# Performance work log

Hardware: AMD Instinct MI355X
Metric: run time of the kernel (lower is better)

Reference implementation:

```python
import jax, jax.numpy as jnp
import numpy as np


def setup_inputs() -> dict:
    key = jax.random.key(0)
    ks = jax.random.split(key, 6)
    L, B, S, D = 2, 32, 2048, 1024
    dec_hidden = jax.random.normal(ks[0], (L, B, D), dtype=jnp.float32)
    enc_out = jax.random.normal(ks[1], (B, S, D), dtype=jnp.float32)
    mask = jax.random.randint(ks[2], (B, S), 0, 2, dtype=jnp.int32)
    sc = 1.0 / np.sqrt(D)
    W_dec = jax.random.normal(ks[3], (D, D), dtype=jnp.float32) * sc
    W_enc = jax.random.normal(ks[4], (D, D), dtype=jnp.float32) * sc
    w_att = jax.random.normal(ks[5], (D, 1), dtype=jnp.float32) * sc
    return {
        "decoder_hidden": dec_hidden,
        "encoder_outputs": enc_out,
        "mask": mask,
        "W_dec": W_dec,
        "b_dec": jnp.zeros((D,), jnp.float32),
        "W_enc": W_enc,
        "b_enc": jnp.zeros((D,), jnp.float32),
        "w_att": w_att,
        "b_att": jnp.zeros((1,), jnp.float32),
    }


def reference(decoder_hidden, encoder_outputs, mask, W_dec, b_dec, W_enc, b_enc, w_att, b_att):
    # decoder_hidden: [L, B, Dd] -> take last layer, project to enc dim: [B, 1, De]
    dec_proj = decoder_hidden[-1] @ W_dec + b_dec            # [B, De]
    enc_proj = jnp.einsum("bse,ef->bsf", encoder_outputs, W_enc) + b_enc  # [B, S, De]
    energy = jnp.tanh(dec_proj[:, None, :] + enc_proj)        # [B, S, De]
    scores = jnp.einsum("bse,eo->bso", energy, w_att)[..., 0] + b_att[0]  # [B, S]
    scores = jnp.where(mask == 0, jnp.float32(-1e10), scores)
    attn = jax.nn.softmax(scores, axis=1)                     # [B, S]
    context = jnp.einsum("bs,bse->be", attn, encoder_outputs)[:, None, :]  # [B, 1, De]
    return context, attn
```

## Files before the change

### kernel.cpp

```cpp
#include <hip/hip_runtime.h>
#include <hip/hip_bf16.h>

constexpr int LAY = 2;
constexpr int BB  = 32;
constexpr int SS  = 2048;
constexpr int DD  = 1024;

typedef unsigned short u16;
typedef short  short8  __attribute__((ext_vector_type(8)));
typedef u16    u16x8   __attribute__((ext_vector_type(8)));
typedef float  floatx4 __attribute__((ext_vector_type(4)));

__device__ inline u16 f2bf_rn(float f) {
    union { float f; unsigned int i; } v; v.f = f;
    unsigned int x = v.i;
    return (u16)((x + 0x7FFFu + ((x >> 16) & 1u)) >> 16);
}

__global__ void transpose_wenc(const float* __restrict__ W, u16* __restrict__ wT) {
    int idx = blockIdx.x * 256 + threadIdx.x;
    int k = idx >> 10, n = idx & 1023;
    wT[n * DD + k] = f2bf_rn(W[idx]);
}

__global__ __launch_bounds__(256) void dec_proj_kernel(
    const float* __restrict__ dec_hidden, const float* __restrict__ W_dec,
    const float* __restrict__ b_dec, float* __restrict__ dec_proj) {
    int b = blockIdx.x, t = threadIdx.x;
    const float* h = dec_hidden + (LAY - 1) * BB * DD + b * DD;
    float acc0 = 0.f, acc1 = 0.f, acc2 = 0.f, acc3 = 0.f;
    for (int e = 0; e < DD; ++e) {
        float hv = h[e];
        const float* wr = W_dec + e * DD;
        acc0 += hv * wr[t];
        acc1 += hv * wr[t + 256];
        acc2 += hv * wr[t + 512];
        acc3 += hv * wr[t + 768];
    }
    float* dp = dec_proj + b * DD;
    dp[t]       = acc0 + b_dec[t];
    dp[t + 256] = acc1 + b_dec[t + 256];
    dp[t + 512] = acc2 + b_dec[t + 512];
    dp[t + 768] = acc3 + b_dec[t + 768];
}

constexpr int LDK = 72;

__global__ __launch_bounds__(256) void score_gemm(
    const float* __restrict__ enc,
    const u16*   __restrict__ wT,
    const float* __restrict__ dec_proj,
    const float* __restrict__ b_enc, const float* __restrict__ w_att,
    float* __restrict__ scores) {
    __shared__ u16 As[128 * LDK];
    __shared__ u16 Bs[128 * LDK];

    const int tid  = threadIdx.x;
    const int bn   = blockIdx.x;
    const int bm   = blockIdx.y;
    const int row0 = bm * 128, col0 = bn * 128;
    const int lane = tid & 63, w = tid >> 6;
    const int wm   = w >> 1,  wn = w & 1;
    const int quad = lane >> 4, l16 = lane & 15;

    const int pr = tid >> 3;
    const int pc = (tid & 7) * 8;

    floatx4 acc[4][4];
    #pragma unroll
    for (int i = 0; i < 4; ++i)
        #pragma unroll
        for (int j = 0; j < 4; ++j)
            acc[i][j] = (floatx4){0.f, 0.f, 0.f, 0.f};

    for (int kt = 0; kt < DD / 64; ++kt) {
        const int k0 = kt * 64;
        floatx4 af0[4], af1[4];
        u16x8 bv[4];
        #pragma unroll
        for (int i = 0; i < 4; ++i) {
            int r = pr + i * 32;
            const float* src = enc + (size_t)(row0 + r) * DD + k0 + pc;
            af0[i] = *reinterpret_cast<const floatx4*>(src);
            af1[i] = *reinterpret_cast<const floatx4*>(src + 4);
            bv[i]  = *reinterpret_cast<const u16x8*>(&wT[(size_t)(col0 + r) * DD + k0 + pc]);
        }
        __syncthreads();
        #pragma unroll
        for (int i = 0; i < 4; ++i) {
            int r = pr + i * 32;
            u16x8 a8;
            #pragma unroll
            for (int j = 0; j < 4; ++j) {
                a8[j]     = f2bf_rn(af0[i][j]);
                a8[4 + j] = f2bf_rn(af1[i][j]);
            }
            *reinterpret_cast<u16x8*>(&As[r * LDK + pc]) = a8;
            *reinterpret_cast<u16x8*>(&Bs[r * LDK + pc]) = bv[i];
        }
        __syncthreads();
        #pragma unroll
        for (int ks = 0; ks < 2; ++ks) {
            short8 a[4], b[4];
            #pragma unroll
            for (int tm = 0; tm < 4; ++tm)
                a[tm] = *reinterpret_cast<const short8*>(
                    &As[(wm * 64 + tm * 16 + l16) * LDK + ks * 32 + quad * 8]);
            #pragma unroll
            for (int tn = 0; tn < 4; ++tn)
                b[tn] = *reinterpret_cast<const short8*>(
                    &Bs[(wn * 64 + tn * 16 + l16) * LDK + ks * 32 + quad * 8]);
            #pragma unroll
            for (int tm = 0; tm < 4; ++tm)
                #pragma unroll
                for (int tn = 0; tn < 4; ++tn)
                    acc[tm][tn] = __builtin_amdgcn_mfma_f32_16x16x32_bf16(
                        a[tm], b[tn], acc[tm][tn], 0, 0, 0);
        }
        __syncthreads();
    }

    const int bIdx = row0 / SS;
    const float* dp = dec_proj + bIdx * DD;
    float cvec[4], wvv[4];
    #pragma unroll
    for (int tn = 0; tn < 4; ++tn) {
        int n = col0 + wn * 64 + tn * 16 + l16;
        cvec[tn] = dp[n] + b_enc[n];
        wvv[tn]  = w_att[n];
    }
    #pragma unroll
    for (int tm = 0; tm < 4; ++tm) {
        float rs0 = 0.f, rs1 = 0.f, rs2 = 0.f, rs3 = 0.f;
        #pragma unroll
        for (int tn = 0; tn < 4; ++tn) {
            rs0 += tanhf(acc[tm][tn][0] + cvec[tn]) * wvv[tn];
            rs1 += tanhf(acc[tm][tn][1] + cvec[tn]) * wvv[tn];
            rs2 += tanhf(acc[tm][tn][2] + cvec[tn]) * wvv[tn];
            rs3 += tanhf(acc[tm][tn][3] + cvec[tn]) * wvv[tn];
        }
        #pragma unroll
        for (int off = 1; off < 16; off <<= 1) {
            rs0 += __shfl_xor(rs0, off, 64);
            rs1 += __shfl_xor(rs1, off, 64);
            rs2 += __shfl_xor(rs2, off, 64);
            rs3 += __shfl_xor(rs3, off, 64);
        }
        if (l16 == 0) {
            int rbase = row0 + wm * 64 + tm * 16 + quad * 4;
            atomicAdd(&scores[rbase + 0], rs0);
            atomicAdd(&scores[rbase + 1], rs1);
            atomicAdd(&scores[rbase + 2], rs2);
            atomicAdd(&scores[rbase + 3], rs3);
        }
    }
}

__global__ __launch_bounds__(256) void softmax_kernel(
    const float* __restrict__ scores, const int* __restrict__ mask,
    float* __restrict__ attn_out) {
    int b = blockIdx.x, t = threadIdx.x;
    const float* srow = scores + b * SS;
    const int*   mrow = mask + b * SS;
    float vals[8];
    float vmax = -1e30f;
    #pragma unroll
    for (int i = 0; i < 8; ++i) {
        int s = i * 256 + t;
        float v = (mrow[s] == 0) ? -1e10f : srow[s];
        vals[i] = v;
        vmax = fmaxf(vmax, v);
    }
    #pragma unroll
    for (int off = 32; off >= 1; off >>= 1) vmax = fmaxf(vmax, __shfl_xor(vmax, off, 64));
    __shared__ float sm[4];
    if ((t & 63) == 0) sm[t >> 6] = vmax;
    __syncthreads();
    vmax = fmaxf(fmaxf(sm[0], sm[1]), fmaxf(sm[2], sm[3]));
    float sum = 0.f;
    #pragma unroll
    for (int i = 0; i < 8; ++i) { vals[i] = __expf(vals[i] - vmax); sum += vals[i]; }
    #pragma unroll
    for (int off = 32; off >= 1; off >>= 1) sum += __shfl_xor(sum, off, 64);
    __shared__ float ssum[4];
    if ((t & 63) == 0) ssum[t >> 6] = sum;
    __syncthreads();
    sum = ssum[0] + ssum[1] + ssum[2] + ssum[3];
    float inv = 1.f / sum;
    #pragma unroll
    for (int i = 0; i < 8; ++i) {
        int s = i * 256 + t;
        attn_out[b * SS + s] = vals[i] * inv;
    }
}

__global__ __launch_bounds__(256) void context_kernel(
    const float* __restrict__ attn, const float* __restrict__ enc,
    float* __restrict__ ctx) {
    int dcb = blockIdx.x;
    int scb = blockIdx.y;
    int b   = blockIdx.z;
    int d = dcb * 256 + threadIdx.x;
    const float* base = enc + ((size_t)b * SS + scb * 256) * DD + d;
    const float* ar   = attn + b * SS + scb * 256;
    float acc = 0.f;
    #pragma unroll 4
    for (int s = 0; s < 256; ++s) acc += ar[s] * base[(size_t)s * DD];
    atomicAdd(&ctx[b * DD + d], acc);
}

extern "C" void kernel_launch(void* const* d_in, const int* in_sizes, int n_in,
                              void* d_out, int out_size, void* d_ws, size_t ws_size,
                              hipStream_t stream) {
    const float* dec_hidden = (const float*)d_in[0];
    const float* enc        = (const float*)d_in[1];
    const int*   mask       = (const int*)d_in[2];
    const float* W_dec      = (const float*)d_in[3];
    const float* b_dec      = (const float*)d_in[4];
    const float* W_enc      = (const float*)d_in[5];
    const float* b_enc      = (const float*)d_in[6];
    const float* w_att      = (const float*)d_in[7];

    float* out = (float*)d_out;
    float* ws  = (float*)d_ws;
    float* dec_proj = ws;
    float* scores   = ws + 32768;
    u16*   wT       = (u16*)(ws + 98304);
    float* attn     = out + 32768;

    hipMemsetAsync(scores, 0, 65536 * sizeof(float), stream);
    hipMemsetAsync(out, 0, 32768 * sizeof(float), stream);

    transpose_wenc<<<4096, 256, 0, stream>>>(W_enc, wT);
    dec_proj_kernel<<<32, 256, 0, stream>>>(dec_hidden, W_dec, b_dec, dec_proj);
    score_gemm<<<dim3(8, 512), 256, 0, stream>>>(enc, wT, dec_proj, b_enc, w_att, scores);
    softmax_kernel<<<32, 256, 0, stream>>>(scores, mask, attn);
    context_kernel<<<dim3(4, 8, 32), 256, 0, stream>>>(attn, enc, out);
}
```

Before: 767.0 us.

## Pre-convert encoder outputs to bf16 and use direct-to-LDS loads in score GEMM

Adds a pass that converts encoder outputs to bf16 once into workspace. The score GEMM then loads bf16 tiles straight into LDS with global_load_lds and no in-loop conversion, and the context kernel reads the bf16 copy. The decoder projection is spread over more blocks. This cuts repeated fp32 reads and per-tile conversion across the 8 column blocks, at the cost of an extra full pass over the encoder tensor and lower precision in the context sum; the old path remains as a fallback when workspace is too small.

```diff
diff --git a/kernel.cpp b/kernel.cpp
--- a/kernel.cpp
+++ b/kernel.cpp
@@ -9,14 +9,34 @@
 typedef unsigned short u16;
 typedef short  short8  __attribute__((ext_vector_type(8)));
 typedef u16    u16x8   __attribute__((ext_vector_type(8)));
+typedef u16    u16x4   __attribute__((ext_vector_type(4)));
 typedef float  floatx4 __attribute__((ext_vector_type(4)));
 
+__device__ inline float bf2f(u16 u) {
+    union { unsigned int i; float f; } v; v.i = ((unsigned int)u) << 16; return v.f;
+}
 __device__ inline u16 f2bf_rn(float f) {
     union { float f; unsigned int i; } v; v.f = f;
     unsigned int x = v.i;
     return (u16)((x + 0x7FFFu + ((x >> 16) & 1u)) >> 16);
 }
 
+__device__ __forceinline__ void gload_lds16(const u16* g, u16* l) {
+    __builtin_amdgcn_global_load_lds(
+        (const __attribute__((address_space(1))) void*)g,
+        (__attribute__((address_space(3))) void*)l, 16, 0, 0);
+}
+
+__global__ __launch_bounds__(256) void convert_enc(const float* __restrict__ enc,
+                                                   u16* __restrict__ encbf) {
+    size_t i = ((size_t)blockIdx.x * 256 + threadIdx.x) * 4;
+    floatx4 v = *reinterpret_cast<const floatx4*>(enc + i);
+    u16x4 r;
+    #pragma unroll
+    for (int j = 0; j < 4; ++j) r[j] = f2bf_rn(v[j]);
+    *reinterpret_cast<u16x4*>(encbf + i) = r;
+}
+
 __global__ void transpose_wenc(const float* __restrict__ W, u16* __restrict__ wT) {
     int idx = blockIdx.x * 256 + threadIdx.x;
     int k = idx >> 10, n = idx & 1023;
@@ -26,34 +46,27 @@
 __global__ __launch_bounds__(256) void dec_proj_kernel(
     const float* __restrict__ dec_hidden, const float* __restrict__ W_dec,
     const float* __restrict__ b_dec, float* __restrict__ dec_proj) {
-    int b = blockIdx.x, t = threadIdx.x;
+    int cb = blockIdx.x, b = blockIdx.y, t = threadIdx.x;
+    int col = cb * 256 + t;
     const float* h = dec_hidden + (LAY - 1) * BB * DD + b * DD;
-    float acc0 = 0.f, acc1 = 0.f, acc2 = 0.f, acc3 = 0.f;
-    for (int e = 0; e < DD; ++e) {
-        float hv = h[e];
-        const float* wr = W_dec + e * DD;
-        acc0 += hv * wr[t];
-        acc1 += hv * wr[t + 256];
-        acc2 += hv * wr[t + 512];
-        acc3 += hv * wr[t + 768];
-    }
-    float* dp = dec_proj + b * DD;
-    dp[t]       = acc0 + b_dec[t];
-    dp[t + 256] = acc1 + b_dec[t + 256];
-    dp[t + 512] = acc2 + b_dec[t + 512];
-    dp[t + 768] = acc3 + b_dec[t + 768];
-}
-
-constexpr int LDK = 72;
-
-__global__ __launch_bounds__(256) void score_gemm(
-    const float* __restrict__ enc,
-    const u16*   __restrict__ wT,
+    float a0 = 0.f, a1 = 0.f, a2 = 0.f, a3 = 0.f;
+    for (int e = 0; e < DD; e += 4) {
+        a0 += h[e + 0] * W_dec[(size_t)(e + 0) * DD + col];
+        a1 += h[e + 1] * W_dec[(size_t)(e + 1) * DD + col];
+        a2 += h[e + 2] * W_dec[(size_t)(e + 2) * DD + col];
+        a3 += h[e + 3] * W_dec[(size_t)(e + 3) * DD + col];
+    }
+    dec_proj[b * DD + col] = (a0 + a1) + (a2 + a3) + b_dec[col];
+}
+
+__global__ __launch_bounds__(256) void score_gemm_bf(
+    const u16* __restrict__ enc,
+    const u16* __restrict__ wT,
     const float* __restrict__ dec_proj,
     const float* __restrict__ b_enc, const float* __restrict__ w_att,
     float* __restrict__ scores) {
-    __shared__ u16 As[128 * LDK];
-    __shared__ u16 Bs[128 * LDK];
+    __shared__ u16 As[128 * 64];
+    __shared__ u16 Bs[128 * 64];
 
     const int tid  = threadIdx.x;
     const int bn   = blockIdx.x;
@@ -63,8 +76,8 @@
     const int wm   = w >> 1,  wn = w & 1;
     const int quad = lane >> 4, l16 = lane & 15;
 
-    const int pr = tid >> 3;
-    const int pc = (tid & 7) * 8;
+    const int srow = w * 8 + (lane >> 3);
+    const int scol = (lane & 7) * 8;
 
     floatx4 acc[4][4];
     #pragma unroll
@@ -72,6 +85,95 @@
         #pragma unroll
         for (int j = 0; j < 4; ++j)
             acc[i][j] = (floatx4){0.f, 0.f, 0.f, 0.f};
+
+    for (int kt = 0; kt < DD / 64; ++kt) {
+        const int k0 = kt * 64;
+        __syncthreads();
+        #pragma unroll
+        for (int i = 0; i < 4; ++i) {
+            gload_lds16(&enc[(size_t)(row0 + i * 32 + srow) * DD + k0 + scol],
+                        &As[(i * 32 + w * 8) * 64]);
+            gload_lds16(&wT [(size_t)(col0 + i * 32 + srow) * DD + k0 + scol],
+                        &Bs[(i * 32 + w * 8) * 64]);
+        }
+        __syncthreads();
+        #pragma unroll
+        for (int ks = 0; ks < 2; ++ks) {
+            short8 a[4], b[4];
+            #pragma unroll
+            for (int tm = 0; tm < 4; ++tm)
+                a[tm] = *reinterpret_cast<const short8*>(
+                    &As[(wm * 64 + tm * 16 + l16) * 64 + ks * 32 + quad * 8]);
+            #pragma unroll
+            for (int tn = 0; tn < 4; ++tn)
+                b[tn] = *reinterpret_cast<const short8*>(
+                    &Bs[(wn * 64 + tn * 16 + l16) * 64 + ks * 32 + quad * 8]);
+            #pragma unroll
+            for (int tm = 0; tm < 4; ++tm)
+                #pragma unroll
+                for (int tn = 0; tn < 4; ++tn)
+                    acc[tm][tn] = __builtin_amdgcn_mfma_f32_16x16x32_bf16(
+                        a[tm], b[tn], acc[tm][tn], 0, 0, 0);
+        }
+    }
+
+    const int bIdx = row0 / SS;
+    const float* dp = dec_proj + bIdx * DD;
+    float cvec[4], wvv[4];
+    #pragma unroll
+    for (int tn = 0; tn < 4; ++tn) {
+        int n = col0 + wn * 64 + tn * 16 + l16;
+        cvec[tn] = dp[n] + b_enc[n];
+        wvv[tn]  = w_att[n];
+    }
+    #pragma unroll
+    for (int tm = 0; tm < 4; ++tm) {
+        float rs0 = 0.f, rs1 = 0.f, rs2 = 0.f, rs3 = 0.f;
+        #pragma unroll
+        for (int tn = 0; tn < 4; ++tn) {
+            rs0 += tanhf(acc[tm][tn][0] + cvec[tn]) * wvv[tn];
+            rs1 += tanhf(acc[tm][tn][1] + cvec[tn]) * wvv[tn];
+            rs2 += tanhf(acc[tm][tn][2] + cvec[tn]) * wvv[tn];
+            rs3 += tanhf(acc[tm][tn][3] + cvec[tn]) * wvv[tn];
+        }
+        #pragma unroll
+        for (int off = 1; off < 16; off <<= 1) {
+            rs0 += __shfl_xor(rs0, off, 64);
+            rs1 += __shfl_xor(rs1, off, 64);
+            rs2 += __shfl_xor(rs2, off, 64);
+            rs3 += __shfl_xor(rs3, off, 64);
+        }
+        if (l16 == 0) {
+            int rbase = row0 + wm * 64 + tm * 16 + quad * 4;
+            atomicAdd(&scores[rbase + 0], rs0);
+            atomicAdd(&scores[rbase + 1], rs1);
+            atomicAdd(&scores[rbase + 2], rs2);
+            atomicAdd(&scores[rbase + 3], rs3);
+        }
+    }
+}
+
+constexpr int LDK2 = 72;
+__global__ __launch_bounds__(256) void score_gemm_f32(
+    const float* __restrict__ enc, const u16* __restrict__ wT,
+    const float* __restrict__ dec_proj,
+    const float* __restrict__ b_enc, const float* __restrict__ w_att,
+    float* __restrict__ scores) {
+    __shared__ u16 As[128 * LDK2];
+    __shared__ u16 Bs[128 * LDK2];
+    const int tid  = threadIdx.x;
+    const int bn   = blockIdx.x, bm = blockIdx.y;
+    const int row0 = bm * 128, col0 = bn * 128;
+    const int lane = tid & 63, w = tid >> 6;
+    const int wm   = w >> 1,  wn = w & 1;
+    const int quad = lane >> 4, l16 = lane & 15;
+    const int pr = tid >> 3, pc = (tid & 7) * 8;
+
+    floatx4 acc[4][4];
+    #pragma unroll
+    for (int i = 0; i < 4; ++i)
+        #pragma unroll
+        for (int j = 0; j < 4; ++j) acc[i][j] = (floatx4){0.f, 0.f, 0.f, 0.f};
 
     for (int kt = 0; kt < DD / 64; ++kt) {
         const int k0 = kt * 64;
@@ -91,12 +193,9 @@
             int r = pr + i * 32;
             u16x8 a8;
             #pragma unroll
-            for (int j = 0; j < 4; ++j) {
-                a8[j]     = f2bf_rn(af0[i][j]);
-                a8[4 + j] = f2bf_rn(af1[i][j]);
-            }
-            *reinterpret_cast<u16x8*>(&As[r * LDK + pc]) = a8;
-            *reinterpret_cast<u16x8*>(&Bs[r * LDK + pc]) = bv[i];
+            for (int j = 0; j < 4; ++j) { a8[j] = f2bf_rn(af0[i][j]); a8[4 + j] = f2bf_rn(af1[i][j]); }
+            *reinterpret_cast<u16x8*>(&As[r * LDK2 + pc]) = a8;
+            *reinterpret_cast<u16x8*>(&Bs[r * LDK2 + pc]) = bv[i];
         }
         __syncthreads();
         #pragma unroll
@@ -105,11 +204,11 @@
             #pragma unroll
             for (int tm = 0; tm < 4; ++tm)
                 a[tm] = *reinterpret_cast<const short8*>(
-                    &As[(wm * 64 + tm * 16 + l16) * LDK + ks * 32 + quad * 8]);
+                    &As[(wm * 64 + tm * 16 + l16) * LDK2 + ks * 32 + quad * 8]);
             #pragma unroll
             for (int tn = 0; tn < 4; ++tn)
                 b[tn] = *reinterpret_cast<const short8*>(
-                    &Bs[(wn * 64 + tn * 16 + l16) * LDK + ks * 32 + quad * 8]);
+                    &Bs[(wn * 64 + tn * 16 + l16) * LDK2 + ks * 32 + quad * 8]);
             #pragma unroll
             for (int tm = 0; tm < 4; ++tm)
                 #pragma unroll
@@ -119,7 +218,6 @@
         }
         __syncthreads();
     }
-
     const int bIdx = row0 / SS;
     const float* dp = dec_proj + bIdx * DD;
     float cvec[4], wvv[4];
@@ -188,18 +286,35 @@
     sum = ssum[0] + ssum[1] + ssum[2] + ssum[3];
     float inv = 1.f / sum;
     #pragma unroll
-    for (int i = 0; i < 8; ++i) {
-        int s = i * 256 + t;
-        attn_out[b * SS + s] = vals[i] * inv;
-    }
-}
-
-__global__ __launch_bounds__(256) void context_kernel(
+    for (int i = 0; i < 8; ++i) attn_out[b * SS + i * 256 + t] = vals[i] * inv;
+}
+
+__global__ __launch_bounds__(256) void context_bf(
+    const float* __restrict__ attn, const u16* __restrict__ encbf,
+    float* __restrict__ ctx) {
+    int scb = blockIdx.x;
+    int b   = blockIdx.y;
+    int d = threadIdx.x * 4;
+    const u16*  base = encbf + ((size_t)b * SS + scb * 256) * DD + d;
+    const float* ar  = attn + b * SS + scb * 256;
+    float a0 = 0.f, a1 = 0.f, a2 = 0.f, a3 = 0.f;
+    #pragma unroll 4
+    for (int s = 0; s < 256; ++s) {
+        u16x4 v = *reinterpret_cast<const u16x4*>(base + (size_t)s * DD);
+        float w = ar[s];
+        a0 += w * bf2f(v[0]); a1 += w * bf2f(v[1]);
+        a2 += w * bf2f(v[2]); a3 += w * bf2f(v[3]);
+    }
+    atomicAdd(&ctx[b * DD + d + 0], a0);
+    atomicAdd(&ctx[b * DD + d + 1], a1);
+    atomicAdd(&ctx[b * DD + d + 2], a2);
+    atomicAdd(&ctx[b * DD + d + 3], a3);
+}
+
+__global__ __launch_bounds__(256) void context_f32(
     const float* __restrict__ attn, const float* __restrict__ enc,
     float* __restrict__ ctx) {
-    int dcb = blockIdx.x;
-    int scb = blockIdx.y;
-    int b   = blockIdx.z;
+    int dcb = blockIdx.x, scb = blockIdx.y, b = blockIdx.z;
     int d = dcb * 256 + threadIdx.x;
     const float* base = enc + ((size_t)b * SS + scb * 256) * DD + d;
     const float* ar   = attn + b * SS + scb * 256;
@@ -226,14 +341,25 @@
     float* dec_proj = ws;
     float* scores   = ws + 32768;
     u16*   wT       = (u16*)(ws + 98304);
+    u16*   encbf    = (u16*)(ws + 622592);
     float* attn     = out + 32768;
+
+    const size_t need = (size_t)622592 * 4 + (size_t)BB * SS * DD * 2;
+    const bool use_bf = ws_size >= need;
 
     hipMemsetAsync(scores, 0, 65536 * sizeof(float), stream);
     hipMemsetAsync(out, 0, 32768 * sizeof(float), stream);
 
     transpose_wenc<<<4096, 256, 0, stream>>>(W_enc, wT);
-    dec_proj_kernel<<<32, 256, 0, stream>>>(dec_hidden, W_dec, b_dec, dec_proj);
-    score_gemm<<<dim3(8, 512), 256, 0, stream>>>(enc, wT, dec_proj, b_enc, w_att, scores);
-    softmax_kernel<<<32, 256, 0, stream>>>(scores, mask, attn);
-    context_kernel<<<dim3(4, 8, 32), 256, 0, stream>>>(attn, enc, out);
-}
+    dec_proj_kernel<<<dim3(4, 32), 256, 0, stream>>>(dec_hidden, W_dec, b_dec, dec_proj);
+    if (use_bf) {
+        convert_enc<<<65536, 256, 0, stream>>>(enc, encbf);
+        score_gemm_bf<<<dim3(8, 512), 256, 0, stream>>>(encbf, wT, dec_proj, b_enc, w_att, scores);
+        softmax_kernel<<<32, 256, 0, stream>>>(scores, mask, attn);
+        context_bf<<<dim3(8, 32), 256, 0, stream>>>(attn, encbf, out);
+    } else {
+        score_gemm_f32<<<dim3(8, 512), 256, 0, stream>>>(enc, wT, dec_proj, b_enc, w_att, scores);
+        softmax_kernel<<<32, 256, 0, stream>>>(scores, mask, attn);
+        context_f32<<<dim3(4, 8, 32), 256, 0, stream>>>(attn, enc, out);
+    }
+}
```

After: 715.6 us. 1.07x faster.

## Pre-convert encoder to bf16, async LDS loads with swizzle, bf16 context pass

Applied to the files above, without the earlier changes.

Adds a pass that converts the fp32 encoder outputs to bf16 once. The score GEMM then streams bf16 tiles straight into LDS with global_load_lds and an XOR-swizzled layout, replacing the per-tile fp32 loads, in-register conversion and padded LDS stores. The context reduction also reads the bf16 copy, halving its traffic but lowering the precision of the context output. W_enc transpose is vectorised and dec_proj is split over K with atomics for more parallelism. The cost is an extra full read and write of the encoder tensor plus a larger workspace.

```diff
diff --git a/kernel.cpp b/kernel.cpp
--- a/kernel.cpp
+++ b/kernel.cpp
@@ -11,49 +11,74 @@
 typedef u16    u16x8   __attribute__((ext_vector_type(8)));
 typedef float  floatx4 __attribute__((ext_vector_type(4)));
 
+__device__ inline float bf2f(u16 u) {
+    union { unsigned int i; float f; } v; v.i = ((unsigned int)u) << 16; return v.f;
+}
 __device__ inline u16 f2bf_rn(float f) {
     union { float f; unsigned int i; } v; v.f = f;
     unsigned int x = v.i;
     return (u16)((x + 0x7FFFu + ((x >> 16) & 1u)) >> 16);
 }
 
-__global__ void transpose_wenc(const float* __restrict__ W, u16* __restrict__ wT) {
-    int idx = blockIdx.x * 256 + threadIdx.x;
-    int k = idx >> 10, n = idx & 1023;
-    wT[n * DD + k] = f2bf_rn(W[idx]);
+__device__ __forceinline__ void gload_lds16(const u16* g, u16* l) {
+    __builtin_amdgcn_global_load_lds(
+        (const __attribute__((address_space(1))) void*)g,
+        (__attribute__((address_space(3))) void*)l, 16, 0, 0);
+}
+
+__global__ __launch_bounds__(256) void convert_enc(const float* __restrict__ enc,
+                                                   u16* __restrict__ encbf) {
+    size_t gid = (size_t)blockIdx.x * 256 + threadIdx.x;
+    #pragma unroll 4
+    for (int it = 0; it < 16; ++it) {
+        size_t i = (it * 524288ull + gid) * 8;
+        floatx4 v0 = *reinterpret_cast<const floatx4*>(enc + i);
+        floatx4 v1 = *reinterpret_cast<const floatx4*>(enc + i + 4);
+        u16x8 r;
+        #pragma unroll
+        for (int j = 0; j < 4; ++j) { r[j] = f2bf_rn(v0[j]); r[4 + j] = f2bf_rn(v1[j]); }
+        *reinterpret_cast<u16x8*>(encbf + i) = r;
+    }
+}
+
+__global__ __launch_bounds__(256) void transpose_wenc(const float* __restrict__ W,
+                                                      u16* __restrict__ wT) {
+    int gid = blockIdx.x * 256 + threadIdx.x;
+    int n = gid & 1023, c = gid >> 10;
+    int k0 = c * 8;
+    u16x8 r;
+    #pragma unroll
+    for (int j = 0; j < 8; ++j) r[j] = f2bf_rn(W[(size_t)(k0 + j) * DD + n]);
+    *reinterpret_cast<u16x8*>(&wT[(size_t)n * DD + k0]) = r;
 }
 
 __global__ __launch_bounds__(256) void dec_proj_kernel(
     const float* __restrict__ dec_hidden, const float* __restrict__ W_dec,
     const float* __restrict__ b_dec, float* __restrict__ dec_proj) {
-    int b = blockIdx.x, t = threadIdx.x;
-    const float* h = dec_hidden + (LAY - 1) * BB * DD + b * DD;
-    float acc0 = 0.f, acc1 = 0.f, acc2 = 0.f, acc3 = 0.f;
-    for (int e = 0; e < DD; ++e) {
-        float hv = h[e];
-        const float* wr = W_dec + e * DD;
-        acc0 += hv * wr[t];
-        acc1 += hv * wr[t + 256];
-        acc2 += hv * wr[t + 512];
-        acc3 += hv * wr[t + 768];
-    }
-    float* dp = dec_proj + b * DD;
-    dp[t]       = acc0 + b_dec[t];
-    dp[t + 256] = acc1 + b_dec[t + 256];
-    dp[t + 512] = acc2 + b_dec[t + 512];
-    dp[t + 768] = acc3 + b_dec[t + 768];
-}
-
-constexpr int LDK = 72;
-
-__global__ __launch_bounds__(256) void score_gemm(
-    const float* __restrict__ enc,
-    const u16*   __restrict__ wT,
+    int kc = blockIdx.x, cb = blockIdx.y, b = blockIdx.z, t = threadIdx.x;
+    int col = cb * 256 + t;
+    const float* h = dec_hidden + (LAY - 1) * BB * DD + b * DD + kc * 256;
+    const float* Wp = W_dec + (size_t)kc * 256 * DD + col;
+    float a0 = 0.f, a1 = 0.f, a2 = 0.f, a3 = 0.f;
+    for (int e = 0; e < 256; e += 4) {
+        a0 += h[e + 0] * Wp[(size_t)(e + 0) * DD];
+        a1 += h[e + 1] * Wp[(size_t)(e + 1) * DD];
+        a2 += h[e + 2] * Wp[(size_t)(e + 2) * DD];
+        a3 += h[e + 3] * Wp[(size_t)(e + 3) * DD];
+    }
+    float v = (a0 + a1) + (a2 + a3);
+    if (kc == 0) v += b_dec[col];
+    atomicAdd(&dec_proj[b * DD + col], v);
+}
+
+__global__ __launch_bounds__(256) void score_gemm_bf(
+    const u16* __restrict__ enc,
+    const u16* __restrict__ wT,
     const float* __restrict__ dec_proj,
     const float* __restrict__ b_enc, const float* __restrict__ w_att,
     float* __restrict__ scores) {
-    __shared__ u16 As[128 * LDK];
-    __shared__ u16 Bs[128 * LDK];
+    __shared__ u16 As[128 * 64];
+    __shared__ u16 Bs[128 * 64];
 
     const int tid  = threadIdx.x;
     const int bn   = blockIdx.x;
@@ -63,8 +88,8 @@
     const int wm   = w >> 1,  wn = w & 1;
     const int quad = lane >> 4, l16 = lane & 15;
 
-    const int pr = tid >> 3;
-    const int pc = (tid & 7) * 8;
+    const int srow = w * 8 + (lane >> 3);
+    const int scol = (((lane & 7) ^ (lane >> 3)) * 8);
 
     floatx4 acc[4][4];
     #pragma unroll
@@ -75,41 +100,30 @@
 
     for (int kt = 0; kt < DD / 64; ++kt) {
         const int k0 = kt * 64;
-        floatx4 af0[4], af1[4];
-        u16x8 bv[4];
+        __syncthreads();
         #pragma unroll
         for (int i = 0; i < 4; ++i) {
-            int r = pr + i * 32;
-            const float* src = enc + (size_t)(row0 + r) * DD + k0 + pc;
-            af0[i] = *reinterpret_cast<const floatx4*>(src);
-            af1[i] = *reinterpret_cast<const floatx4*>(src + 4);
-            bv[i]  = *reinterpret_cast<const u16x8*>(&wT[(size_t)(col0 + r) * DD + k0 + pc]);
-        }
-        __syncthreads();
-        #pragma unroll
-        for (int i = 0; i < 4; ++i) {
-            int r = pr + i * 32;
-            u16x8 a8;
-            #pragma unroll
-            for (int j = 0; j < 4; ++j) {
-                a8[j]     = f2bf_rn(af0[i][j]);
-                a8[4 + j] = f2bf_rn(af1[i][j]);
-            }
-            *reinterpret_cast<u16x8*>(&As[r * LDK + pc]) = a8;
-            *reinterpret_cast<u16x8*>(&Bs[r * LDK + pc]) = bv[i];
+            gload_lds16(&enc[(size_t)(row0 + i * 32 + srow) * DD + k0 + scol],
+                        &As[(i * 32 + w * 8) * 64]);
+            gload_lds16(&wT [(size_t)(col0 + i * 32 + srow) * DD + k0 + scol],
+                        &Bs[(i * 32 + w * 8) * 64]);
         }
         __syncthreads();
         #pragma unroll
         for (int ks = 0; ks < 2; ++ks) {
             short8 a[4], b[4];
             #pragma unroll
-            for (int tm = 0; tm < 4; ++tm)
-                a[tm] = *reinterpret_cast<const short8*>(
-                    &As[(wm * 64 + tm * 16 + l16) * LDK + ks * 32 + quad * 8]);
+            for (int tm = 0; tm < 4; ++tm) {
+                int r = wm * 64 + tm * 16 + l16;
+                int kcs = (ks * 4 + quad) ^ (l16 & 7);
+                a[tm] = *reinterpret_cast<const short8*>(&As[r * 64 + kcs * 8]);
+            }
             #pragma unroll
-            for (int tn = 0; tn < 4; ++tn)
-                b[tn] = *reinterpret_cast<const short8*>(
-                    &Bs[(wn * 64 + tn * 16 + l16) * LDK + ks * 32 + quad * 8]);
+            for (int tn = 0; tn < 4; ++tn) {
+                int r = wn * 64 + tn * 16 + l16;
+                int kcs = (ks * 4 + quad) ^ (l16 & 7);
+                b[tn] = *reinterpret_cast<const short8*>(&Bs[r * 64 + kcs * 8]);
+            }
             #pragma unroll
             for (int tm = 0; tm < 4; ++tm)
                 #pragma unroll
@@ -117,7 +131,6 @@
                     acc[tm][tn] = __builtin_amdgcn_mfma_f32_16x16x32_bf16(
                         a[tm], b[tn], acc[tm][tn], 0, 0, 0);
         }
-        __syncthreads();
     }
 
     const int bIdx = row0 / SS;
@@ -188,25 +201,32 @@
     sum = ssum[0] + ssum[1] + ssum[2] + ssum[3];
     float inv = 1.f / sum;
     #pragma unroll
-    for (int i = 0; i < 8; ++i) {
-        int s = i * 256 + t;
-        attn_out[b * SS + s] = vals[i] * inv;
-    }
-}
-
-__global__ __launch_bounds__(256) void context_kernel(
-    const float* __restrict__ attn, const float* __restrict__ enc,
+    for (int i = 0; i < 8; ++i) attn_out[b * SS + i * 256 + t] = vals[i] * inv;
+}
+
+__global__ __launch_bounds__(256) void context_bf(
+    const float* __restrict__ attn, const u16* __restrict__ encbf,
     float* __restrict__ ctx) {
-    int dcb = blockIdx.x;
-    int scb = blockIdx.y;
-    int b   = blockIdx.z;
-    int d = dcb * 256 + threadIdx.x;
-    const float* base = enc + ((size_t)b * SS + scb * 256) * DD + d;
-    const float* ar   = attn + b * SS + scb * 256;
-    float acc = 0.f;
+    int scb = blockIdx.x;
+    int b   = blockIdx.y;
+    int d = threadIdx.x * 4;
+    const u16*  base = encbf + ((size_t)b * SS + scb * 256) * DD + d;
+    const float* ar  = attn + b * SS + scb * 256;
+    float a0 = 0.f, a1 = 0.f, a2 = 0.f, a3 = 0.f;
     #pragma unroll 4
-    for (int s = 0; s < 256; ++s) acc += ar[s] * base[(size_t)s * DD];
-    atomicAdd(&ctx[b * DD + d], acc);
+    for (int s = 0; s < 256; ++s) {
+        u16x8 dummy; (void)dummy;
+        unsigned long long v = *reinterpret_cast<const unsigned long long*>(base + (size_t)s * DD);
+        float w = ar[s];
+        a0 += w * bf2f((u16)(v       & 0xFFFF));
+        a1 += w * bf2f((u16)((v >> 16) & 0xFFFF));
+        a2 += w * bf2f((u16)((v >> 32) & 0xFFFF));
+        a3 += w * bf2f((u16)((v >> 48) & 0xFFFF));
+    }
+    atomicAdd(&ctx[b * DD + d + 0], a0);
+    atomicAdd(&ctx[b * DD + d + 1], a1);
+    atomicAdd(&ctx[b * DD + d + 2], a2);
+    atomicAdd(&ctx[b * DD + d + 3], a3);
 }
 
 extern "C" void kernel_launch(void* const* d_in, const int* in_sizes, int n_in,
@@ -226,14 +246,16 @@
     float* dec_proj = ws;
     float* scores   = ws + 32768;
     u16*   wT       = (u16*)(ws + 98304);
+    u16*   encbf    = (u16*)(ws + 622592);
     float* attn     = out + 32768;
 
-    hipMemsetAsync(scores, 0, 65536 * sizeof(float), stream);
+    hipMemsetAsync(ws, 0, 98304 * sizeof(float), stream);
     hipMemsetAsync(out, 0, 32768 * sizeof(float), stream);
 
-    transpose_wenc<<<4096, 256, 0, stream>>>(W_enc, wT);
-    dec_proj_kernel<<<32, 256, 0, stream>>>(dec_hidden, W_dec, b_dec, dec_proj);
-    score_gemm<<<dim3(8, 512), 256, 0, stream>>>(enc, wT, dec_proj, b_enc, w_att, scores);
+    convert_enc<<<2048, 256, 0, stream>>>(enc, encbf);
+    transpose_wenc<<<512, 256, 0, stream>>>(W_enc, wT);
+    dec_proj_kernel<<<dim3(4, 4, 32), 256, 0, stream>>>(dec_hidden, W_dec, b_dec, dec_proj);
+    score_gemm_bf<<<dim3(8, 512), 256, 0, stream>>>(encbf, wT, dec_proj, b_enc, w_att, scores);
     softmax_kernel<<<32, 256, 0, stream>>>(scores, mask, attn);
-    context_kernel<<<dim3(4, 8, 32), 256, 0, stream>>>(attn, enc, out);
-}
+    context_bf<<<dim3(8, 32), 256, 0, stream>>>(attn, encbf, out);
+}
```

Result: faster. 696.1 us (-9.2%).
